# Optimization experiments

Hardware: AMD Instinct MI355X
Metric: run time of the kernel (lower is better)

## Reference

```python
import jax, jax.numpy as jnp
import numpy as np
from jax import lax

K = 3            # kernel size
KP = K * K       # kernel_size_prod
CENTER = KP // 2 # center tap index
PIXEL_SIZE = 1.0
DILATION = 1


def _unfold(x):
    # torch F.unfold equivalent: [N, C*KP, oh, ow] with channel-major, spatial-minor tap order
    return lax.conv_general_dilated_patches(
        x, filter_shape=(K, K), window_strides=(1, 1),
        padding=((1, 1), (1, 1)), rhs_dilation=(DILATION, DILATION))


def setup_inputs() -> dict:
    key = jax.random.key(0)
    ks = jax.random.split(key, 6)
    N, C, O, H, W = 8, 128, 128, 64, 64
    x = jax.random.normal(ks[0], (N, C, H, W), jnp.float32)
    depth = jax.random.uniform(ks[1], (N, 1, H, W), jnp.float32)  # >0 almost surely
    fx = jax.random.uniform(ks[2], (N,), jnp.float32) + 0.5       # per-image focal scale
    s = 1.0 / np.sqrt(C * KP)
    w0 = jax.random.normal(ks[3], (O, C, K, K), jnp.float32) * s
    w1 = jax.random.normal(ks[4], (O, C, K, K), jnp.float32) * s
    w2 = jax.random.normal(ks[5], (O, C, K, K), jnp.float32) * s
    return {"x": x, "depth": depth, "fx": fx, "w0": w0, "w1": w1, "w2": w2}


def reference(x, depth, fx, w0, w1, w2):
    N, C, H, W = x.shape
    O = w0.shape[0]
    patches = _unfold(x)                      # [N, C*9, oh, ow]
    oh, ow = patches.shape[2], patches.shape[3]
    L = oh * ow
    x_col = patches.reshape(N, C, KP, L)       # [N, C, 9, L]
    d_col = _unfold(depth).reshape(N, KP, L)   # [N, 9, L]

    valid = (d_col != 0.0).astype(jnp.float32)
    valid = valid * valid[:, CENTER:CENTER + 1, :]
    d_col = d_col * valid
    center = d_col[:, CENTER:CENTER + 1, :]    # [N, 1, L]
    grid = PIXEL_SIZE * DILATION * center / fx[:, None, None]
    half = grid * 0.5

    m0 = (jnp.abs(d_col - (center + grid)) <= half).astype(jnp.float32)
    m1 = (jnp.abs(d_col - center) <= half).astype(jnp.float32)
    m1 = jnp.clip(m1 + 1.0 - valid, 0.0, 1.0)
    m2 = (jnp.abs(d_col - (center - grid)) <= half).astype(jnp.float32)

    def branch(w, m):
        # (O, C*9) @ (N, C*9, L) as an einsum over (C, tap)
        return jnp.einsum('ock,nckl->nol', w.reshape(O, C, KP), x_col * m[:, None])

    out = branch(w0, m0) + branch(w1, m1) + branch(w2, m2)
    return out.reshape(N, O, oh, ow)
```

## Files before the change

### kernel.cpp

```cpp
#include <hip/hip_runtime.h>
#include <hip/hip_bf16.h>
#include <cstdint>
#include <cstddef>

#define Nn 8
#define Cc 128
#define Oo 128
#define Hh 64
#define Ww 64
#define LL (Hh * Ww)
#define KP 9

typedef __attribute__((ext_vector_type(8))) short short8;
typedef __attribute__((ext_vector_type(4))) float floatx4;
typedef __attribute__((ext_vector_type(16))) float f32x16;
typedef __attribute__((ext_vector_type(4))) int intx4;

__device__ __forceinline__ unsigned short f2bf(float f) {
  unsigned int u = __float_as_uint(f);
  u += 0x7fffu + ((u >> 16) & 1u);
  return (unsigned short)(u >> 16);
}

__global__ __launch_bounds__(256) void prep_all(const float* __restrict__ x,
                                                const float* __restrict__ w0,
                                                const float* __restrict__ w1,
                                                const float* __restrict__ w2,
                                                const float* __restrict__ depth,
                                                const float* __restrict__ fx,
                                                unsigned short* __restrict__ xt,
                                                unsigned short* __restrict__ wt2,
                                                unsigned int* __restrict__ codesg) {
  __shared__ float tile[Cc][Ww + 1];
  __shared__ unsigned short wl[Cc * KP];
  const int bid = blockIdx.x;
  const int t = threadIdx.x;
  if (bid < Nn * Hh) {
    const int n = bid >> 6;
    const int h = bid & 63;
    const float* src = x + (size_t)n * Cc * LL + (size_t)h * Ww;
#pragma unroll
    for (int it = 0; it < 8; ++it) {
      const int idx = t + it * 256;
      const int c = idx >> 4;
      const int w4 = (idx & 15) << 2;
      const float4 v = *reinterpret_cast<const float4*>(src + (size_t)c * LL + w4);
      tile[c][w4 + 0] = v.x; tile[c][w4 + 1] = v.y;
      tile[c][w4 + 2] = v.z; tile[c][w4 + 3] = v.w;
    }
    __syncthreads();
    unsigned short* dst = xt + (size_t)((n * Hh + h) * Ww) * Cc;
#pragma unroll
    for (int it = 0; it < 4; ++it) {
      const int idx = t + it * 256;
      const int w = idx >> 4;
      const int ch = (idx & 15) << 3;
      short8 v;
#pragma unroll
      for (int q = 0; q < 8; ++q)
        ((unsigned short*)&v)[q] = f2bf(tile[ch + q][w]);
      *reinterpret_cast<short8*>(dst + (size_t)w * Cc + ch) = v;
    }
  } else if (bid < Nn * Hh + 3 * Oo) {
    const int bo = bid - Nn * Hh;
    const int b = bo >> 7;
    const int o = bo & 127;
    const float* w = (b == 0) ? w0 : (b == 1) ? w1 : w2;
    const float* src = w + (size_t)o * Cc * KP;
#pragma unroll
    for (int it = 0; it < 5; ++it) {
      const int idx = t + it * 256;
      if (idx < Cc * KP) wl[idx] = f2bf(src[idx]);
    }
    __syncthreads();
#pragma unroll
    for (int it = 0; it < 5; ++it) {
      const int idx = t + it * 256;
      if (idx < Cc * KP) {
        const int kk = idx >> 7;
        const int c = idx & 127;
        wt2[(size_t)(((b * 9 + kk) * 16 + (c >> 3)) * 128 + o) * 8 + (c & 7)] =
            wl[c * KP + kk];
      }
    }
  } else {
    const int p = (bid - (Nn * Hh + 3 * Oo)) * 256 + t;
    const int n = p >> 12;
    const int rem = p & 4095;
    const int h = rem >> 6;
    const int w = rem & 63;
    const float center = depth[p];
    const float grid = center / fx[n];
    const float half = 0.5f * grid;
    unsigned int packed = 0u;
#pragma unroll
    for (int kk = 0; kk < KP; ++kk) {
      const int hh = h + kk / 3 - 1;
      const int ww = w + kk % 3 - 1;
      float d = 0.0f;
      if (hh >= 0 && hh < Hh && ww >= 0 && ww < Ww) d = depth[(n << 12) + hh * Ww + ww];
      const float valid = (d != 0.0f && center != 0.0f) ? 1.0f : 0.0f;
      const float dm = d * valid;
      unsigned int cb = 0u;
      if (fabsf(dm - (center + grid)) <= half) cb |= 1u;
      float m1v = (fabsf(dm - center) <= half) ? 1.0f : 0.0f;
      m1v = m1v + 1.0f - valid;
      if (m1v > 1.0f) m1v = 1.0f;
      if (m1v > 0.5f) cb |= 2u;
      if (fabsf(dm - (center - grid)) <= half) cb |= 4u;
      packed |= cb << (3 * kk);
    }
    codesg[p] = packed;
  }
}

#define LDXC 132
#define HALO_COLS 66
#define HALO_ROWS 4

__global__ __launch_bounds__(256, 2) void conv_main(
    const unsigned short* __restrict__ xt,
    const unsigned short* __restrict__ wt2,
    const unsigned int* __restrict__ codesg,
    float* __restrict__ out) {
  __shared__ __align__(16) unsigned short Xs[HALO_ROWS * HALO_COLS * LDXC];

  const int g = blockIdx.x;
  const int n = g >> 6;
  const int rem = g & 63;
  const int pb = rem >> 1;
  const int ob1 = rem & 1;
  const int h0 = pb * 2;

  const int tid = threadIdx.x;
  const int lane = tid & 63;
  const int wave = tid >> 6;
  const int l31 = lane & 31;
  const int lg = lane >> 5;
  const int wc = wave & 1;
  const int ks = wave >> 1;

  const unsigned short* wf =
      wt2 + ((size_t)(ks * 8 + lg) * 128 + ob1 * 64 + wc * 32 + l31) * 8;

  short8 Bb[2][6];
  short8 Aa[2][8];

#define LOADB(SLOT, KK, HF)                                                          \
  {                                                                                  \
    const int kkq = (KK), hfq = (HF);                                                \
    _Pragma("unroll")                                                                \
    for (int kc = 0; kc < 2; ++kc)                                                   \
      _Pragma("unroll")                                                              \
      for (int b = 0; b < 3; ++b)                                                    \
        Bb[SLOT][kc * 3 + b] = *reinterpret_cast<const short8*>(                     \
            wf + (size_t)(((b * 9 + kkq) * 16 + hfq * 4 + kc * 2)) * 1024);          \
  }

#define LOADA(SLOT, KK, HF)                                                          \
  {                                                                                  \
    const int kkp = (KK), hfp = (HF);                                                \
    const int dyp = kkp / 3, dxp = kkp - dyp * 3;                                    \
    const int pof = dyp * HALO_COLS + dxp + l31;                                     \
    _Pragma("unroll")                                                                \
    for (int mt = 0; mt < 4; ++mt)                                                   \
      _Pragma("unroll")                                                              \
      for (int kc = 0; kc < 2; ++kc) {                                               \
        const int pix = (mt >> 1) * HALO_COLS + (mt & 1) * 32 + pof;                 \
        const int coff = ks * 64 + hfp * 32 + kc * 16 + lg * 8;                      \
        Aa[SLOT][mt * 2 + kc] =                                                      \
            *reinterpret_cast<const short8*>(&Xs[pix * LDXC + coff]);                \
      }                                                                              \
  }

#define COMPUTE(BSLOT, ASLOT, KK)                                                    \
  {                                                                                  \
    const int shift = 3 * (KK);                                                      \
    _Pragma("unroll")                                                                \
    for (int b = 0; b < 3; ++b) {                                                    \
      int msk[4];                                                                    \
      _Pragma("unroll")                                                              \
      for (int mt = 0; mt < 4; ++mt)                                                 \
        msk[mt] = __builtin_amdgcn_sbfe((int)cd2[mt], shift + b, 1);                 \
      _Pragma("unroll")                                                              \
      for (int kc = 0; kc < 2; ++kc) {                                               \
        _Pragma("unroll")                                                            \
        for (int mt = 0; mt < 4; ++mt) {                                             \
          intx4 a4 = *reinterpret_cast<const intx4*>(&Aa[ASLOT][mt * 2 + kc]);       \
          intx4 m4 = {msk[mt], msk[mt], msk[mt], msk[mt]};                           \
          a4 &= m4;                                                                  \
          const short8 af = *reinterpret_cast<const short8*>(&a4);                   \
          acc2[mt] = __builtin_amdgcn_mfma_f32_32x32x16_bf16(                        \
              af, Bb[BSLOT][kc * 3 + b], acc2[mt], 0, 0, 0);                         \
        }                                                                            \
      }                                                                              \
    }                                                                                \
  }

  LOADB(0, 0, 0)
  LOADB(1, 0, 1)

  unsigned int cd2[4];
  {
    const unsigned int* cp = codesg + (n << 12) + h0 * 64;
#pragma unroll
    for (int mt = 0; mt < 4; ++mt) cd2[mt] = cp[mt * 32 + l31];
  }

#pragma unroll
  for (int it = 0; it < 17; ++it) {
    const int idx = tid + it * 256;
    if (idx < HALO_ROWS * HALO_COLS * 16) {
      const int ch = (idx & 15) << 3;
      const int pixidx = idx >> 4;
      const int lc = pixidx % HALO_COLS;
      const int hrel = pixidx / HALO_COLS;
      const int hh = h0 - 1 + hrel;
      const int ww = lc - 1;
      short8 v = {0, 0, 0, 0, 0, 0, 0, 0};
      if (hh >= 0 && hh < Hh && ww >= 0 && ww < Ww)
        v = *reinterpret_cast<const short8*>(
            xt + (size_t)((n * Hh + hh) * Ww + ww) * Cc + ch);
      *reinterpret_cast<short8*>(&Xs[pixidx * LDXC + ch]) = v;
    }
  }

  __syncthreads();

  f32x16 acc2[4];
#pragma unroll
  for (int mt = 0; mt < 4; ++mt)
    acc2[mt] = (f32x16){0.f, 0.f, 0.f, 0.f, 0.f, 0.f, 0.f, 0.f,
                        0.f, 0.f, 0.f, 0.f, 0.f, 0.f, 0.f, 0.f};

  LOADA(0, 0, 0)

#pragma unroll 1
  for (int p = 0; p < 8; ++p) {
    LOADA(1, p, 1)
    COMPUTE(0, 0, p)
    LOADB(0, p + 1, 0)
    LOADA(0, p + 1, 0)
    COMPUTE(1, 1, p)
    LOADB(1, p + 1, 1)
  }
  LOADA(1, 8, 1)
  COMPUTE(0, 0, 8)
  COMPUTE(1, 1, 8)

  __syncthreads();
  float* scratch = reinterpret_cast<float*>(Xs);
  if (ks == 1) {
#pragma unroll
    for (int mt = 0; mt < 4; ++mt)
#pragma unroll
      for (int q4 = 0; q4 < 4; ++q4) {
        const floatx4 v = {acc2[mt][q4 * 4 + 0], acc2[mt][q4 * 4 + 1],
                           acc2[mt][q4 * 4 + 2], acc2[mt][q4 * 4 + 3]};
        *reinterpret_cast<floatx4*>(
            &scratch[(((wc * 4 + mt) * 4 + q4) * 64 + lane) * 4]) = v;
      }
  }
  __syncthreads();
  if (ks == 0) {
    const int o = ob1 * 64 + wc * 32 + l31;
#pragma unroll
    for (int mt = 0; mt < 4; ++mt) {
      const int h = h0 + (mt >> 1);
      const int wbase = (mt & 1) * 32;
#pragma unroll
      for (int q4 = 0; q4 < 4; ++q4) {
        const floatx4 other = *reinterpret_cast<const floatx4*>(
            &scratch[(((wc * 4 + mt) * 4 + q4) * 64 + lane) * 4]);
        const floatx4 mine = {acc2[mt][q4 * 4 + 0], acc2[mt][q4 * 4 + 1],
                              acc2[mt][q4 * 4 + 2], acc2[mt][q4 * 4 + 3]};
        const floatx4 sum = mine + other;
        const int w = wbase + q4 * 8 + lg * 4;
        float* dst = out + (size_t)(n * Oo + o) * LL + h * Ww + w;
        *reinterpret_cast<floatx4*>(dst) = sum;
      }
    }
  }
}

extern "C" void kernel_launch(void* const* d_in, const int* in_sizes, int n_in,
                              void* d_out, int out_size, void* d_ws, size_t ws_size,
                              hipStream_t stream) {
  const float* x     = (const float*)d_in[0];
  const float* depth = (const float*)d_in[1];
  const float* fx    = (const float*)d_in[2];
  const float* w0    = (const float*)d_in[3];
  const float* w1    = (const float*)d_in[4];
  const float* w2    = (const float*)d_in[5];
  float* out = (float*)d_out;

  unsigned short* xt = (unsigned short*)d_ws;
  unsigned short* wt2 = xt + (size_t)Nn * Hh * Ww * Cc;
  unsigned int* codesg = (unsigned int*)(wt2 + (size_t)3 * KP * Oo * Cc);

  prep_all<<<Nn * Hh + 3 * Oo + 128, 256, 0, stream>>>(x, w0, w1, w2, depth, fx, xt, wt2, codesg);
  conv_main<<<512, 256, 0, stream>>>(xt, wt2, codesg, out);
}
```

Baseline: 110.2 us.

## Split channel reduction across four wave pairs with 512-thread blocks

Doubles the block to 512 threads (8 waves) and splits the 128-channel reduction into four 32-channel slices instead of two 64-channel slices, so each wave holds half the A/B fragments and issues half the MFMAs per tap. Partial accumulators are then combined in two stages through shared memory. The aim is more waves in flight to hide LDS and global-load latency, and fewer registers per thread. The cost is an extra shared-memory reduction pass with added barriers, plus more instructions per MFMA for the loads.

```diff
diff --git a/kernel.cpp b/kernel.cpp
--- a/kernel.cpp
+++ b/kernel.cpp
@@ -118,7 +118,7 @@
 #define HALO_COLS 66
 #define HALO_ROWS 4
 
-__global__ __launch_bounds__(256, 2) void conv_main(
+__global__ __launch_bounds__(512, 4) void conv_main(
     const unsigned short* __restrict__ xt,
     const unsigned short* __restrict__ wt2,
     const unsigned int* __restrict__ codesg,
@@ -141,20 +141,18 @@
   const int ks = wave >> 1;
 
   const unsigned short* wf =
-      wt2 + ((size_t)(ks * 8 + lg) * 128 + ob1 * 64 + wc * 32 + l31) * 8;
-
-  short8 Bb[2][6];
-  short8 Aa[2][8];
+      wt2 + ((size_t)(ks * 4 + lg) * 128 + ob1 * 64 + wc * 32 + l31) * 8;
+
+  short8 Bb[2][3];
+  short8 Aa[2][4];
 
 #define LOADB(SLOT, KK, HF)                                                          \
   {                                                                                  \
     const int kkq = (KK), hfq = (HF);                                                \
     _Pragma("unroll")                                                                \
-    for (int kc = 0; kc < 2; ++kc)                                                   \
-      _Pragma("unroll")                                                              \
-      for (int b = 0; b < 3; ++b)                                                    \
-        Bb[SLOT][kc * 3 + b] = *reinterpret_cast<const short8*>(                     \
-            wf + (size_t)(((b * 9 + kkq) * 16 + hfq * 4 + kc * 2)) * 1024);          \
+    for (int b = 0; b < 3; ++b)                                                      \
+      Bb[SLOT][b] = *reinterpret_cast<const short8*>(                                \
+          wf + (size_t)((b * 9 + kkq) * 16 + hfq * 2) * 1024);                       \
   }
 
 #define LOADA(SLOT, KK, HF)                                                          \
@@ -162,15 +160,12 @@
     const int kkp = (KK), hfp = (HF);                                                \
     const int dyp = kkp / 3, dxp = kkp - dyp * 3;                                    \
     const int pof = dyp * HALO_COLS + dxp + l31;                                     \
+    const int coff = ks * 32 + hfp * 16 + lg * 8;                                    \
     _Pragma("unroll")                                                                \
-    for (int mt = 0; mt < 4; ++mt)                                                   \
-      _Pragma("unroll")                                                              \
-      for (int kc = 0; kc < 2; ++kc) {                                               \
-        const int pix = (mt >> 1) * HALO_COLS + (mt & 1) * 32 + pof;                 \
-        const int coff = ks * 64 + hfp * 32 + kc * 16 + lg * 8;                      \
-        Aa[SLOT][mt * 2 + kc] =                                                      \
-            *reinterpret_cast<const short8*>(&Xs[pix * LDXC + coff]);                \
-      }                                                                              \
+    for (int mt = 0; mt < 4; ++mt) {                                                 \
+      const int pix = (mt >> 1) * HALO_COLS + (mt & 1) * 32 + pof;                   \
+      Aa[SLOT][mt] = *reinterpret_cast<const short8*>(&Xs[pix * LDXC + coff]);       \
+    }                                                                                \
   }
 
 #define COMPUTE(BSLOT, ASLOT, KK)                                                    \
@@ -178,21 +173,15 @@
     const int shift = 3 * (KK);                                                      \
     _Pragma("unroll")                                                                \
     for (int b = 0; b < 3; ++b) {                                                    \
-      int msk[4];                                                                    \
       _Pragma("unroll")                                                              \
-      for (int mt = 0; mt < 4; ++mt)                                                 \
-        msk[mt] = __builtin_amdgcn_sbfe((int)cd2[mt], shift + b, 1);                 \
-      _Pragma("unroll")                                                              \
-      for (int kc = 0; kc < 2; ++kc) {                                               \
-        _Pragma("unroll")                                                            \
-        for (int mt = 0; mt < 4; ++mt) {                                             \
-          intx4 a4 = *reinterpret_cast<const intx4*>(&Aa[ASLOT][mt * 2 + kc]);       \
-          intx4 m4 = {msk[mt], msk[mt], msk[mt], msk[mt]};                           \
-          a4 &= m4;                                                                  \
-          const short8 af = *reinterpret_cast<const short8*>(&a4);                   \
-          acc2[mt] = __builtin_amdgcn_mfma_f32_32x32x16_bf16(                        \
-              af, Bb[BSLOT][kc * 3 + b], acc2[mt], 0, 0, 0);                         \
-        }                                                                            \
+      for (int mt = 0; mt < 4; ++mt) {                                               \
+        const int msk = __builtin_amdgcn_sbfe((int)cd2[mt], shift + b, 1);           \
+        intx4 a4 = *reinterpret_cast<const intx4*>(&Aa[ASLOT][mt]);                  \
+        intx4 m4 = {msk, msk, msk, msk};                                             \
+        a4 &= m4;                                                                    \
+        const short8 af = *reinterpret_cast<const short8*>(&a4);                     \
+        acc2[mt] = __builtin_amdgcn_mfma_f32_32x32x16_bf16(                          \
+            af, Bb[BSLOT][b], acc2[mt], 0, 0, 0);                                    \
       }                                                                              \
     }                                                                                \
   }
@@ -208,8 +197,8 @@
   }
 
 #pragma unroll
-  for (int it = 0; it < 17; ++it) {
-    const int idx = tid + it * 256;
+  for (int it = 0; it < 9; ++it) {
+    const int idx = tid + it * 512;
     if (idx < HALO_ROWS * HALO_COLS * 16) {
       const int ch = (idx & 15) << 3;
       const int pixidx = idx >> 4;
@@ -250,6 +239,34 @@
 
   __syncthreads();
   float* scratch = reinterpret_cast<float*>(Xs);
+  if (ks >= 2) {
+    const int region = ks - 2;
+#pragma unroll
+    for (int mt = 0; mt < 4; ++mt)
+#pragma unroll
+      for (int q4 = 0; q4 < 4; ++q4) {
+        const floatx4 v = {acc2[mt][q4 * 4 + 0], acc2[mt][q4 * 4 + 1],
+                           acc2[mt][q4 * 4 + 2], acc2[mt][q4 * 4 + 3]};
+        *reinterpret_cast<floatx4*>(
+            &scratch[region * 8192 + (((wc * 4 + mt) * 4 + q4) * 64 + lane) * 4]) = v;
+      }
+  }
+  __syncthreads();
+  if (ks < 2) {
+    const int region = ks;
+#pragma unroll
+    for (int mt = 0; mt < 4; ++mt)
+#pragma unroll
+      for (int q4 = 0; q4 < 4; ++q4) {
+        const floatx4 other = *reinterpret_cast<const floatx4*>(
+            &scratch[region * 8192 + (((wc * 4 + mt) * 4 + q4) * 64 + lane) * 4]);
+        acc2[mt][q4 * 4 + 0] += other[0];
+        acc2[mt][q4 * 4 + 1] += other[1];
+        acc2[mt][q4 * 4 + 2] += other[2];
+        acc2[mt][q4 * 4 + 3] += other[3];
+      }
+  }
+  __syncthreads();
   if (ks == 1) {
 #pragma unroll
     for (int mt = 0; mt < 4; ++mt)
@@ -299,5 +316,5 @@
   unsigned int* codesg = (unsigned int*)(wt2 + (size_t)3 * KP * Oo * Cc);
 
   prep_all<<<Nn * Hh + 3 * Oo + 128, 256, 0, stream>>>(x, w0, w1, w2, depth, fx, xt, wt2, codesg);
-  conv_main<<<512, 256, 0, stream>>>(xt, wt2, codesg, out);
+  conv_main<<<512, 512, 0, stream>>>(xt, wt2, codesg, out);
 }
```

Result: no change. 111.1 us (+0.8%).
